# Optimization experiments

Hardware: AMD Instinct MI355X
Metric: run time of the kernel (lower is better)

The kernel has to match this reference:

```python
import jax, jax.numpy as jnp
import numpy as np

WH, WW = 7, 7
DIM, HEADS = 256, 8


def make_table_index(wh, ww):
    # relative coords table (log-spaced CPB input) and relative position index
    ch = np.arange(-(wh - 1), wh, dtype=np.float32)
    cw = np.arange(-(ww - 1), ww, dtype=np.float32)
    t = np.stack(np.meshgrid(ch, cw, indexing='ij'), axis=-1)[None]  # [1,2wh-1,2ww-1,2]
    t = t.copy()
    t[..., 0] /= (wh - 1)
    t[..., 1] /= (ww - 1)
    t *= 8.0
    t = np.sign(t) * np.log2(np.abs(t) + 1.0) / np.log2(8.0)
    coords = np.stack(np.meshgrid(np.arange(wh), np.arange(ww), indexing='ij'))
    cf = coords.reshape(2, -1)
    rc = (cf[:, :, None] - cf[:, None, :]).transpose(1, 2, 0).copy()  # [N,N,2]
    rc[..., 0] += wh - 1
    rc[..., 1] += ww - 1
    rc[..., 0] *= 2 * ww - 1
    idx = rc.sum(-1)
    return t.astype(np.float32), idx.astype(np.int32)


def setup_inputs() -> dict:
    key = jax.random.key(0)
    ks = jax.random.split(key, 10)
    B_, N, C, H = 2048, WH * WW, DIM, HEADS
    table, idx = make_table_index(WH, WW)
    return {
        'x': jax.random.normal(ks[0], (B_, N, C), jnp.float32),
        'mask': jnp.zeros((64, N, N), jnp.float32),
        'qkv_w': jax.random.normal(ks[1], (3 * C, C), jnp.float32) * 0.02,
        'q_bias': jnp.zeros((C,), jnp.float32),
        'v_bias': jnp.zeros((C,), jnp.float32),
        'logit_scale': jnp.full((H, 1, 1), np.log(10.0), jnp.float32),
        'cpb_w1': jax.random.normal(ks[2], (512, 2), jnp.float32) * 0.02,
        'cpb_b1': jnp.zeros((512,), jnp.float32),
        'cpb_w2': jax.random.normal(ks[3], (H, 512), jnp.float32) * 0.02,
        'proj_w': jax.random.normal(ks[4], (C, C), jnp.float32) * 0.02,
        'proj_b': jnp.zeros((C,), jnp.float32),
        'rel_coords_table': jnp.asarray(table),
        'rel_pos_index': jnp.asarray(idx),
    }


def _l2norm(t):
    return t / jnp.maximum(jnp.linalg.norm(t, axis=-1, keepdims=True), 1e-12)


def reference(x, mask, qkv_w, q_bias, v_bias, logit_scale, cpb_w1, cpb_b1,
              cpb_w2, proj_w, proj_b, rel_coords_table, rel_pos_index):
    B_, N, C = x.shape
    H = logit_scale.shape[0]
    hd = C // H
    qkv_b = jnp.concatenate([q_bias, jnp.zeros_like(v_bias), v_bias])
    qkv = (x @ qkv_w.T + qkv_b).reshape(B_, N, 3, H, hd).transpose(2, 0, 3, 1, 4)
    q, k, v = qkv[0], qkv[1], qkv[2]  # [B_,H,N,hd]
    attn = jnp.einsum('bhnd,bhmd->bhnm', _l2norm(q), _l2norm(k))
    scale = jnp.exp(jnp.minimum(logit_scale, jnp.log(jnp.float32(100.0))))  # [H,1,1]
    attn = attn * scale[None]
    # CPB MLP -> relative position bias
    table = jax.nn.relu(rel_coords_table @ cpb_w1.T + cpb_b1) @ cpb_w2.T  # [1,Th,Tw,H]
    table = table.reshape(-1, H)
    bias = table[rel_pos_index.reshape(-1)].reshape(N, N, H).transpose(2, 0, 1)
    attn = attn + 16.0 * jax.nn.sigmoid(bias)[None]
    nW = mask.shape[0]
    attn = attn.reshape(B_ // nW, nW, H, N, N) + mask[None, :, None]
    attn = jax.nn.softmax(attn.reshape(B_, H, N, N), axis=-1)
    out = jnp.einsum('bhnm,bhmd->bhnd', attn, v).transpose(0, 2, 1, 3).reshape(B_, N, C)
    return out @ proj_w.T + proj_b
```

## Files before the change

kernel.cpp:

```cpp
#include <hip/hip_runtime.h>

#define DEV __device__ __forceinline__

typedef float  f32x4  __attribute__((ext_vector_type(4)));
typedef __bf16 bf16x8 __attribute__((ext_vector_type(8)));

DEV unsigned short f2bf(float f) {
  unsigned u = __float_as_uint(f);
  u += 0x7fffu + ((u >> 16) & 1u);
  return (unsigned short)(u >> 16);
}
DEV float bf2f(unsigned short v) { return __uint_as_float(((unsigned)v) << 16); }

DEV void cp16(const void* g, void* l) {
  __builtin_amdgcn_global_load_lds((const __attribute__((address_space(1))) void*)g,
                                   (__attribute__((address_space(3))) void*)l, 16, 0, 0);
}

__global__ __launch_bounds__(256) void prep_kernel(
    const float* __restrict__ qkv_w, const float* __restrict__ proj_w,
    const float* __restrict__ q_bias, const float* __restrict__ v_bias,
    unsigned short* __restrict__ wq, unsigned short* __restrict__ wp,
    float* __restrict__ qkvb)
{
  int gid = blockIdx.x * 256 + threadIdx.x;
  if (gid < 196608) wq[gid] = f2bf(qkv_w[gid]);
  else              wp[gid - 196608] = f2bf(proj_w[gid - 196608]);
  if (gid < 768)
    qkvb[gid] = (gid < 256) ? q_bias[gid] : ((gid < 512) ? 0.f : v_bias[gid - 512]);
}

__global__ __launch_bounds__(64) void cpb_mlp(
    const float* __restrict__ tab, const float* __restrict__ w1,
    const float* __restrict__ b1, const float* __restrict__ w2,
    float* __restrict__ table16)
{
  int r = blockIdx.x;
  int t = threadIdx.x;
  float x0 = tab[r * 2 + 0], x1 = tab[r * 2 + 1];
  float part[8];
#pragma unroll
  for (int h = 0; h < 8; ++h) part[h] = 0.f;
  for (int j = t; j < 512; j += 64) {
    float hv = fmaxf(w1[j * 2 + 0] * x0 + w1[j * 2 + 1] * x1 + b1[j], 0.f);
#pragma unroll
    for (int h = 0; h < 8; ++h) part[h] += hv * w2[h * 512 + j];
  }
#pragma unroll
  for (int h = 0; h < 8; ++h) {
    float v = part[h];
    for (int off = 32; off > 0; off >>= 1) v += __shfl_down(v, off, 64);
    if (t == 0) table16[r * 8 + h] = 16.f / (1.f + expf(-v));
  }
}

__global__ __launch_bounds__(256) void bmb(
    const float* __restrict__ t16, const int* __restrict__ ridx,
    const float* __restrict__ mask, float* __restrict__ bias64,
    float* __restrict__ mask64)
{
  int gid = blockIdx.x * 256 + threadIdx.x;
  int p = gid & 4095, i = p >> 6, j = p & 63;
  bool valid = (i < 49) && (j < 49);
  if (gid < 32768) {
    int h = gid >> 12;
    bias64[gid] = valid ? t16[ridx[i * 49 + j] * 8 + h] : 0.f;
  } else {
    int g2 = gid - 32768;
    int w = g2 >> 12;
    mask64[g2] = valid ? mask[w * 2401 + i * 49 + j] : 0.f;
  }
}

__global__ __launch_bounds__(256) void gemm_qkv(
    const float* __restrict__ X, const unsigned short* __restrict__ W,
    const float* __restrict__ bias, unsigned short* __restrict__ qkv)
{
  __shared__ __align__(1024) unsigned short sA[128 * 64];
  __shared__ __align__(1024) unsigned short sB[128 * 64];
  const int t = threadIdx.x, w = t >> 6, l = t & 63, quad = l >> 4, l15 = l & 15;
  const int idx = blockIdx.x;
  const int x8 = idx & 7, local = idx >> 3;
  const int my = x8 * 98 + local / 6, bnb = local % 6;
  const int bm = my * 128, bn = bnb * 128;
  const int wm = (w >> 1) * 64, wn = (w & 1) * 64;
  const int arow = t >> 1, ahalf = t & 1;
  const int srow = t >> 3, sch = t & 7;

  f32x4 acc[4][4] = {};
#pragma unroll 1
  for (int kt = 0; kt < 4; ++kt) {
    const int k0 = kt << 6;
    if (kt) __syncthreads();
#pragma unroll
    for (int i = 0; i < 4; ++i) {
      const int row = i * 32 + srow;
      const int sc  = sch ^ (srow & 7);
      cp16(W + (size_t)(bn + row) * 256 + k0 + sc * 8, sB + (i * 256 + w * 64) * 8);
    }
    {
      const float* ap = X + (size_t)(bm + arow) * 256 + k0 + ahalf * 32;
#pragma unroll
      for (int c = 0; c < 4; ++c) {
        float4 f0 = *(const float4*)(ap + c * 8);
        float4 f1 = *(const float4*)(ap + c * 8 + 4);
        uint4 u;
        u.x = f2bf(f0.x) | ((unsigned)f2bf(f0.y) << 16);
        u.y = f2bf(f0.z) | ((unsigned)f2bf(f0.w) << 16);
        u.z = f2bf(f1.x) | ((unsigned)f2bf(f1.y) << 16);
        u.w = f2bf(f1.z) | ((unsigned)f2bf(f1.w) << 16);
        const int cb = ahalf * 4 + c;
        *(uint4*)&sA[arow * 64 + ((cb ^ (arow & 7)) * 8)] = u;
      }
    }
    __syncthreads();
#pragma unroll
    for (int kk = 0; kk < 2; ++kk) {
      bf16x8 xf[4], wf[4];
#pragma unroll
      for (int mt = 0; mt < 4; ++mt)
        xf[mt] = *(const bf16x8*)&sA[(wm + mt * 16 + l15) * 64 + (((4 * kk + quad) ^ (l15 & 7)) * 8)];
#pragma unroll
      for (int nt = 0; nt < 4; ++nt)
        wf[nt] = *(const bf16x8*)&sB[(wn + nt * 16 + l15) * 64 + (((4 * kk + quad) ^ (l15 & 7)) * 8)];
#pragma unroll
      for (int nt = 0; nt < 4; ++nt)
#pragma unroll
        for (int mt = 0; mt < 4; ++mt)
          acc[nt][mt] = __builtin_amdgcn_mfma_f32_16x16x32_bf16(wf[nt], xf[mt], acc[nt][mt], 0, 0, 0);
    }
  }
  const int nbase = bn + wn;
#pragma unroll
  for (int mA = 0; mA < 4; ++mA) {
    const int mrow = bm + wm + mA * 16 + l15;
    const unsigned bb = (unsigned)(((unsigned long long)mrow * 87652394ull) >> 32);
    const int tok = mrow - (int)bb * 49;
#pragma unroll
    for (int k = 0; k < 2; ++k) {
      const int n0 = nbase + k * 32;
      const int s = n0 >> 8, h = (n0 >> 5) & 7;
      const f32x4 b0 = *(const f32x4*)(bias + n0 + quad * 4);
      const f32x4 b1 = *(const f32x4*)(bias + n0 + 16 + quad * 4);
      const f32x4 a0 = acc[2 * k][mA], a1 = acc[2 * k + 1][mA];
      uint4 u;
      u.x = f2bf(a0[0] + b0[0]) | ((unsigned)f2bf(a0[1] + b0[1]) << 16);
      u.y = f2bf(a0[2] + b0[2]) | ((unsigned)f2bf(a0[3] + b0[3]) << 16);
      u.z = f2bf(a1[0] + b1[0]) | ((unsigned)f2bf(a1[1] + b1[1]) << 16);
      u.w = f2bf(a1[2] + b1[2]) | ((unsigned)f2bf(a1[3] + b1[3]) << 16);
      *(uint4*)(qkv + (size_t)((bb * 8u + h) * 3u + s) * 1568 + tok * 32 + quad * 8) = u;
    }
  }
}

__global__ __launch_bounds__(256) void attn2(
    const unsigned short* __restrict__ qkv, const float* __restrict__ logit_scale,
    const float* __restrict__ bias64, const float* __restrict__ mask64,
    unsigned short* __restrict__ aout)
{
  __shared__ __align__(1024) char smem[4 * 12544];
  const int w = threadIdx.x >> 6, l = threadIdx.x & 63, quad = l >> 4, l15 = l & 15;
  const int flat = blockIdx.x * 4 + w;
  const int b = flat >> 3, h = flat & 7;
  char* my = smem + w * 12544;
  unsigned short* vT = (unsigned short*)my;
  unsigned short* P  = (unsigned short*)(my + 4096);
  float* rk = (float*)(my + 12288);

  const unsigned short* qb = qkv + (size_t)flat * 4704;
  const unsigned short* kb = qb + 1568;
  const unsigned short* vb = qb + 3136;

  bf16x8 kf[4], qf[4];
#pragma unroll
  for (int mt = 0; mt < 4; ++mt) kf[mt] = *(const bf16x8*)(kb + (mt * 16 + l15) * 32 + quad * 8);
#pragma unroll
  for (int nt = 0; nt < 4; ++nt) qf[nt] = *(const bf16x8*)(qb + (nt * 16 + l15) * 32 + quad * 8);

  const float scale = __expf(fminf(logit_scale[h], 4.60517019f));
  float rqv[4];
#pragma unroll
  for (int nt = 0; nt < 4; ++nt) {
    float s = 0.f;
#pragma unroll
    for (int d = 0; d < 8; ++d) { float f = (float)qf[nt][d]; s += f * f; }
    s += __shfl_xor(s, 16, 64); s += __shfl_xor(s, 32, 64);
    rqv[nt] = scale / fmaxf(sqrtf(s), 1e-12f);
  }
#pragma unroll
  for (int mt = 0; mt < 4; ++mt) {
    float s = 0.f;
#pragma unroll
    for (int d = 0; d < 8; ++d) { float f = (float)kf[mt][d]; s += f * f; }
    s += __shfl_xor(s, 16, 64); s += __shfl_xor(s, 32, 64);
    if (quad == 0) rk[mt * 16 + l15] = 1.f / fmaxf(sqrtf(s), 1e-12f);
  }

  if (l < 49) {
    unsigned short vv[32];
#pragma unroll
    for (int c = 0; c < 4; ++c) *(uint4*)&vv[c * 8] = *(const uint4*)(vb + l * 32 + c * 8);
#pragma unroll
    for (int dp = 0; dp < 32; ++dp) {
      const int d = (((dp >> 2) & 1) << 4) + ((dp >> 3) << 2) + (dp & 3);
      vT[d * 64 + (((l >> 3) ^ (d & 7)) << 3) + (l & 7)] = vv[dp];
    }
  } else {
#pragma unroll
    for (int d = 0; d < 32; ++d)
      vT[d * 64 + (((l >> 3) ^ (d & 7)) << 3) + (l & 7)] = 0;
  }
  __syncthreads();

  f32x4 acc[4][4] = {};
#pragma unroll
  for (int mt = 0; mt < 4; ++mt)
#pragma unroll
    for (int nt = 0; nt < 4; ++nt)
      acc[mt][nt] = __builtin_amdgcn_mfma_f32_16x16x32_bf16(kf[mt], qf[nt], acc[mt][nt], 0, 0, 0);

  const float* bh = bias64 + (size_t)h * 4096;
  const float* mw = mask64 + (size_t)(b & 63) * 4096;
#pragma unroll
  for (int nt = 0; nt < 4; ++nt) {
    const int i = nt * 16 + l15;
    const float rqi = rqv[nt];
    float s[4][4];
    float mx = -1e30f;
#pragma unroll
    for (int mt = 0; mt < 4; ++mt) {
      const int jb = mt * 16 + quad * 4;
      const f32x4 b4  = *(const f32x4*)(bh + i * 64 + jb);
      const f32x4 m4  = *(const f32x4*)(mw + i * 64 + jb);
      const f32x4 rk4 = *(const f32x4*)(rk + jb);
#pragma unroll
      for (int r = 0; r < 4; ++r) {
        float sv = acc[mt][nt][r] * (rqi * rk4[r]) + b4[r] + m4[r];
        sv = (jb + r < 49) ? sv : -1e30f;
        s[mt][r] = sv;
        mx = fmaxf(mx, sv);
      }
    }
    mx = fmaxf(mx, __shfl_xor(mx, 16, 64));
    mx = fmaxf(mx, __shfl_xor(mx, 32, 64));
    float sum = 0.f;
    float p[4][4];
#pragma unroll
    for (int mt = 0; mt < 4; ++mt)
#pragma unroll
      for (int r = 0; r < 4; ++r) {
        float pv = __expf(s[mt][r] - mx);
        p[mt][r] = pv; sum += pv;
      }
    sum += __shfl_xor(sum, 16, 64);
    sum += __shfl_xor(sum, 32, 64);
    const float rs = 1.f / sum;
#pragma unroll
    for (int mt = 0; mt < 4; ++mt) {
      unsigned d0 = f2bf(p[mt][0] * rs) | ((unsigned)f2bf(p[mt][1] * rs) << 16);
      unsigned d1 = f2bf(p[mt][2] * rs) | ((unsigned)f2bf(p[mt][3] * rs) << 16);
      const int c = 2 * mt + (quad >> 1);
      uint2 uv; uv.x = d0; uv.y = d1;
      *(uint2*)((char*)P + i * 128 + ((c ^ (i & 7)) * 16) + (quad & 1) * 8) = uv;
    }
  }
  __syncthreads();

  f32x4 oacc[2][4] = {};
#pragma unroll
  for (int kk = 0; kk < 2; ++kk) {
    bf16x8 vf[2], pf[4];
#pragma unroll
    for (int mt = 0; mt < 2; ++mt)
      vf[mt] = *(const bf16x8*)((char*)vT + (mt * 16 + l15) * 128 + (((4 * kk + quad) ^ (l15 & 7)) * 16));
#pragma unroll
    for (int nt = 0; nt < 4; ++nt)
      pf[nt] = *(const bf16x8*)((char*)P + (nt * 16 + l15) * 128 + (((4 * kk + quad) ^ (l15 & 7)) * 16));
#pragma unroll
    for (int mt = 0; mt < 2; ++mt)
#pragma unroll
      for (int nt = 0; nt < 4; ++nt)
        oacc[mt][nt] = __builtin_amdgcn_mfma_f32_16x16x32_bf16(vf[mt], pf[nt], oacc[mt][nt], 0, 0, 0);
  }

#pragma unroll
  for (int nt = 0; nt < 4; ++nt) {
    const int tok = nt * 16 + l15;
    if (tok < 49) {
      unsigned short* op = aout + (size_t)(b * 49 + tok) * 256 + h * 32;
#pragma unroll
      for (int mt = 0; mt < 2; ++mt) {
        unsigned u0 = f2bf(oacc[mt][nt][0]) | ((unsigned)f2bf(oacc[mt][nt][1]) << 16);
        unsigned u1 = f2bf(oacc[mt][nt][2]) | ((unsigned)f2bf(oacc[mt][nt][3]) << 16);
        uint2 uv; uv.x = u0; uv.y = u1;
        *(uint2*)(op + mt * 16 + quad * 4) = uv;
      }
    }
  }
}

__global__ __launch_bounds__(256) void gemm_proj(
    const unsigned short* __restrict__ A, const unsigned short* __restrict__ W,
    const float* __restrict__ bias, float* __restrict__ Y)
{
  __shared__ __align__(1024) unsigned short sA[128 * 64];
  __shared__ __align__(1024) unsigned short sB[128 * 64];
  const int t = threadIdx.x, w = t >> 6, l = t & 63, quad = l >> 4, l15 = l & 15;
  const int bm = blockIdx.y * 128, bn = blockIdx.x * 128;
  const int wm = (w >> 1) * 64, wn = (w & 1) * 64;
  const int srow = t >> 3, sch = t & 7;

  f32x4 acc[4][4] = {};
  for (int kt = 0; kt < 4; ++kt) {
    const int k0 = kt << 6;
    if (kt) __syncthreads();
#pragma unroll
    for (int i = 0; i < 4; ++i) {
      const int row = i * 32 + srow;
      const int sc  = sch ^ (srow & 7);
      cp16(A + (size_t)(bm + row) * 256 + k0 + sc * 8, sA + (i * 256 + w * 64) * 8);
      cp16(W + (size_t)(bn + row) * 256 + k0 + sc * 8, sB + (i * 256 + w * 64) * 8);
    }
    __syncthreads();
#pragma unroll
    for (int kk = 0; kk < 2; ++kk) {
      bf16x8 xf[4], wf[4];
#pragma unroll
      for (int mt = 0; mt < 4; ++mt)
        xf[mt] = *(const bf16x8*)&sA[(wm + mt * 16 + l15) * 64 + (((4 * kk + quad) ^ (l15 & 7)) * 8)];
#pragma unroll
      for (int nt = 0; nt < 4; ++nt)
        wf[nt] = *(const bf16x8*)&sB[(wn + nt * 16 + l15) * 64 + (((4 * kk + quad) ^ (l15 & 7)) * 8)];
#pragma unroll
      for (int nt = 0; nt < 4; ++nt)
#pragma unroll
        for (int mt = 0; mt < 4; ++mt)
          acc[nt][mt] = __builtin_amdgcn_mfma_f32_16x16x32_bf16(wf[nt], xf[mt], acc[nt][mt], 0, 0, 0);
    }
  }
#pragma unroll
  for (int mA = 0; mA < 4; ++mA) {
    const int row = bm + wm + mA * 16 + l15;
    float* orow = Y + (size_t)row * 256;
#pragma unroll
    for (int nW = 0; nW < 4; ++nW) {
      const int c0 = bn + wn + nW * 16 + quad * 4;
      const f32x4 bv = *(const f32x4*)(bias + c0);
      f32x4 v = acc[nW][mA];
      v[0] += bv[0]; v[1] += bv[1]; v[2] += bv[2]; v[3] += bv[3];
      *(f32x4*)(orow + c0) = v;
    }
  }
}

extern "C" void kernel_launch(void* const* d_in, const int* in_sizes, int n_in,
                              void* d_out, int out_size, void* d_ws, size_t ws_size,
                              hipStream_t stream) {
  const float* x           = (const float*)d_in[0];
  const float* mask        = (const float*)d_in[1];
  const float* qkv_w       = (const float*)d_in[2];
  const float* q_bias      = (const float*)d_in[3];
  const float* v_bias      = (const float*)d_in[4];
  const float* logit_scale = (const float*)d_in[5];
  const float* cpb_w1      = (const float*)d_in[6];
  const float* cpb_b1      = (const float*)d_in[7];
  const float* cpb_w2      = (const float*)d_in[8];
  const float* proj_w      = (const float*)d_in[9];
  const float* proj_b      = (const float*)d_in[10];
  const float* rel_tab     = (const float*)d_in[11];
  const int*   rel_idx     = (const int*)d_in[12];
  float*       out         = (float*)d_out;

  char* ws = (char*)d_ws;
  unsigned short* qkvp    = (unsigned short*)(ws + 0);
  unsigned short* aows    = (unsigned short*)(ws + 154140672);
  unsigned short* wq      = (unsigned short*)(ws + 205520896);
  unsigned short* wp      = (unsigned short*)(ws + 205914112);
  float*          qkvb    = (float*)(ws + 206045184);
  float*          table16 = (float*)(ws + 206048256);
  float*          bias64  = (float*)(ws + 206053888);
  float*          mask64  = (float*)(ws + 206184960);

  prep_kernel<<<1024, 256, 0, stream>>>(qkv_w, proj_w, q_bias, v_bias, wq, wp, qkvb);
  cpb_mlp<<<169, 64, 0, stream>>>(rel_tab, cpb_w1, cpb_b1, cpb_w2, table16);
  bmb<<<1152, 256, 0, stream>>>(table16, rel_idx, mask, bias64, mask64);
  gemm_qkv<<<4704, 256, 0, stream>>>(x, wq, qkvb, qkvp);
  attn2<<<4096, 256, 0, stream>>>(qkvp, logit_scale, bias64, mask64, aows);
  gemm_proj<<<dim3(2, 784), 256, 0, stream>>>(aows, wp, proj_b, out);
}
```

Before: 413.4 us.

## Double-buffer LDS tiles in QKV and projection GEMMs to overlap loads with MFMA

Both GEMM kernels switch to two LDS buffers per operand. The next K-tile is prefetched (global_load_lds for weights and A, register prefetch of fp32 X in the QKV GEMM) while MFMAs run on the current tile. Explicit s_waitcnt vmcnt counts and sched barriers replace the __syncthreads pairs. This hides global-load latency behind compute, at the cost of double the LDS footprint, which may lower occupancy, and a fragile hand-set wait count.

```diff
diff --git a/kernel.cpp b/kernel.cpp
--- a/kernel.cpp
+++ b/kernel.cpp
@@ -76,8 +76,8 @@
     const float* __restrict__ X, const unsigned short* __restrict__ W,
     const float* __restrict__ bias, unsigned short* __restrict__ qkv)
 {
-  __shared__ __align__(1024) unsigned short sA[128 * 64];
-  __shared__ __align__(1024) unsigned short sB[128 * 64];
+  __shared__ __align__(1024) unsigned short sA[2][128 * 64];
+  __shared__ __align__(1024) unsigned short sB[2][128 * 64];
   const int t = threadIdx.x, w = t >> 6, l = t & 63, quad = l >> 4, l15 = l & 15;
   const int idx = blockIdx.x;
   const int x8 = idx & 7, local = idx >> 3;
@@ -86,49 +86,71 @@
   const int wm = (w >> 1) * 64, wn = (w & 1) * 64;
   const int arow = t >> 1, ahalf = t & 1;
   const int srow = t >> 3, sch = t & 7;
+  const int sc = sch ^ (srow & 7);
+
+  const unsigned short* wsrc = W + (size_t)(bn + srow) * 256 + sc * 8;
+  const float*          abase = X + (size_t)(bm + arow) * 256 + ahalf * 32;
+
+  float4 areg[8];
+
+  auto issueB = [&](int kt, int buf) {
+#pragma unroll
+    for (int i = 0; i < 4; ++i)
+      cp16(wsrc + (size_t)i * 32 * 256 + (kt << 6), &sB[buf][(i * 256 + w * 64) * 8]);
+  };
+  auto loadA = [&](int kt) {
+    const float* ap = abase + (kt << 6);
+#pragma unroll
+    for (int c = 0; c < 4; ++c) {
+      areg[2 * c]     = *(const float4*)(ap + c * 8);
+      areg[2 * c + 1] = *(const float4*)(ap + c * 8 + 4);
+    }
+  };
+  auto writeA = [&](int buf) {
+#pragma unroll
+    for (int c = 0; c < 4; ++c) {
+      float4 f0 = areg[2 * c], f1 = areg[2 * c + 1];
+      uint4 u;
+      u.x = f2bf(f0.x) | ((unsigned)f2bf(f0.y) << 16);
+      u.y = f2bf(f0.z) | ((unsigned)f2bf(f0.w) << 16);
+      u.z = f2bf(f1.x) | ((unsigned)f2bf(f1.y) << 16);
+      u.w = f2bf(f1.z) | ((unsigned)f2bf(f1.w) << 16);
+      const int cb = ahalf * 4 + c;
+      *(uint4*)&sA[buf][arow * 64 + ((cb ^ (arow & 7)) * 8)] = u;
+    }
+  };
 
   f32x4 acc[4][4] = {};
-#pragma unroll 1
+  issueB(0, 0);
+  loadA(0);
+#pragma unroll
   for (int kt = 0; kt < 4; ++kt) {
-    const int k0 = kt << 6;
-    if (kt) __syncthreads();
-#pragma unroll
-    for (int i = 0; i < 4; ++i) {
-      const int row = i * 32 + srow;
-      const int sc  = sch ^ (srow & 7);
-      cp16(W + (size_t)(bn + row) * 256 + k0 + sc * 8, sB + (i * 256 + w * 64) * 8);
-    }
-    {
-      const float* ap = X + (size_t)(bm + arow) * 256 + k0 + ahalf * 32;
-#pragma unroll
-      for (int c = 0; c < 4; ++c) {
-        float4 f0 = *(const float4*)(ap + c * 8);
-        float4 f1 = *(const float4*)(ap + c * 8 + 4);
-        uint4 u;
-        u.x = f2bf(f0.x) | ((unsigned)f2bf(f0.y) << 16);
-        u.y = f2bf(f0.z) | ((unsigned)f2bf(f0.w) << 16);
-        u.z = f2bf(f1.x) | ((unsigned)f2bf(f1.y) << 16);
-        u.w = f2bf(f1.z) | ((unsigned)f2bf(f1.w) << 16);
-        const int cb = ahalf * 4 + c;
-        *(uint4*)&sA[arow * 64 + ((cb ^ (arow & 7)) * 8)] = u;
-      }
-    }
-    __syncthreads();
+    const int cur = kt & 1;
+    writeA(cur);
+    if (kt < 3) { issueB(kt + 1, cur ^ 1); loadA(kt + 1); }
+    if (kt < 3) asm volatile("s_waitcnt vmcnt(12) lgkmcnt(0)" ::: "memory");
+    else        asm volatile("s_waitcnt vmcnt(0) lgkmcnt(0)" ::: "memory");
+    __builtin_amdgcn_sched_barrier(0);
+    __builtin_amdgcn_s_barrier();
+    __builtin_amdgcn_sched_barrier(0);
 #pragma unroll
     for (int kk = 0; kk < 2; ++kk) {
       bf16x8 xf[4], wf[4];
 #pragma unroll
       for (int mt = 0; mt < 4; ++mt)
-        xf[mt] = *(const bf16x8*)&sA[(wm + mt * 16 + l15) * 64 + (((4 * kk + quad) ^ (l15 & 7)) * 8)];
+        xf[mt] = *(const bf16x8*)&sA[cur][(wm + mt * 16 + l15) * 64 + (((4 * kk + quad) ^ (l15 & 7)) * 8)];
 #pragma unroll
       for (int nt = 0; nt < 4; ++nt)
-        wf[nt] = *(const bf16x8*)&sB[(wn + nt * 16 + l15) * 64 + (((4 * kk + quad) ^ (l15 & 7)) * 8)];
+        wf[nt] = *(const bf16x8*)&sB[cur][(wn + nt * 16 + l15) * 64 + (((4 * kk + quad) ^ (l15 & 7)) * 8)];
 #pragma unroll
       for (int nt = 0; nt < 4; ++nt)
 #pragma unroll
         for (int mt = 0; mt < 4; ++mt)
           acc[nt][mt] = __builtin_amdgcn_mfma_f32_16x16x32_bf16(wf[nt], xf[mt], acc[nt][mt], 0, 0, 0);
     }
+    __builtin_amdgcn_sched_barrier(0);
+    __builtin_amdgcn_s_barrier();
+    __builtin_amdgcn_sched_barrier(0);
   }
   const int nbase = bn + wn;
 #pragma unroll
@@ -303,40 +325,53 @@
     const unsigned short* __restrict__ A, const unsigned short* __restrict__ W,
     const float* __restrict__ bias, float* __restrict__ Y)
 {
-  __shared__ __align__(1024) unsigned short sA[128 * 64];
-  __shared__ __align__(1024) unsigned short sB[128 * 64];
+  __shared__ __align__(1024) unsigned short sA[2][128 * 64];
+  __shared__ __align__(1024) unsigned short sB[2][128 * 64];
   const int t = threadIdx.x, w = t >> 6, l = t & 63, quad = l >> 4, l15 = l & 15;
   const int bm = blockIdx.y * 128, bn = blockIdx.x * 128;
   const int wm = (w >> 1) * 64, wn = (w & 1) * 64;
   const int srow = t >> 3, sch = t & 7;
+  const int sc = sch ^ (srow & 7);
+  const unsigned short* asrc = A + (size_t)(bm + srow) * 256 + sc * 8;
+  const unsigned short* wsrc = W + (size_t)(bn + srow) * 256 + sc * 8;
+
+  auto stage = [&](int kt, int buf) {
+#pragma unroll
+    for (int i = 0; i < 4; ++i) {
+      cp16(asrc + (size_t)i * 32 * 256 + (kt << 6), &sA[buf][(i * 256 + w * 64) * 8]);
+      cp16(wsrc + (size_t)i * 32 * 256 + (kt << 6), &sB[buf][(i * 256 + w * 64) * 8]);
+    }
+  };
 
   f32x4 acc[4][4] = {};
+  stage(0, 0);
+#pragma unroll
   for (int kt = 0; kt < 4; ++kt) {
-    const int k0 = kt << 6;
-    if (kt) __syncthreads();
-#pragma unroll
-    for (int i = 0; i < 4; ++i) {
-      const int row = i * 32 + srow;
-      const int sc  = sch ^ (srow & 7);
-      cp16(A + (size_t)(bm + row) * 256 + k0 + sc * 8, sA + (i * 256 + w * 64) * 8);
-      cp16(W + (size_t)(bn + row) * 256 + k0 + sc * 8, sB + (i * 256 + w * 64) * 8);
-    }
-    __syncthreads();
+    const int cur = kt & 1;
+    if (kt < 3) stage(kt + 1, cur ^ 1);
+    if (kt < 3) asm volatile("s_waitcnt vmcnt(8)" ::: "memory");
+    else        asm volatile("s_waitcnt vmcnt(0)" ::: "memory");
+    __builtin_amdgcn_sched_barrier(0);
+    __builtin_amdgcn_s_barrier();
+    __builtin_amdgcn_sched_barrier(0);
 #pragma unroll
     for (int kk = 0; kk < 2; ++kk) {
       bf16x8 xf[4], wf[4];
 #pragma unroll
       for (int mt = 0; mt < 4; ++mt)
-        xf[mt] = *(const bf16x8*)&sA[(wm + mt * 16 + l15) * 64 + (((4 * kk + quad) ^ (l15 & 7)) * 8)];
+        xf[mt] = *(const bf16x8*)&sA[cur][(wm + mt * 16 + l15) * 64 + (((4 * kk + quad) ^ (l15 & 7)) * 8)];
 #pragma unroll
       for (int nt = 0; nt < 4; ++nt)
-        wf[nt] = *(const bf16x8*)&sB[(wn + nt * 16 + l15) * 64 + (((4 * kk + quad) ^ (l15 & 7)) * 8)];
+        wf[nt] = *(const bf16x8*)&sB[cur][(wn + nt * 16 + l15) * 64 + (((4 * kk + quad) ^ (l15 & 7)) * 8)];
 #pragma unroll
       for (int nt = 0; nt < 4; ++nt)
 #pragma unroll
         for (int mt = 0; mt < 4; ++mt)
           acc[nt][mt] = __builtin_amdgcn_mfma_f32_16x16x32_bf16(wf[nt], xf[mt], acc[nt][mt], 0, 0, 0);
     }
+    __builtin_amdgcn_sched_barrier(0);
+    __builtin_amdgcn_s_barrier();
+    __builtin_amdgcn_sched_barrier(0);
   }
 #pragma unroll
   for (int mA = 0; mA < 4; ++mA) {
```

Measured after the change: 429.4 us. +3.9%, slower.
